# Performance work log

Hardware: AMD Instinct MI355X
Metric: run time of the kernel (lower is better)

The kernel has to match this reference:

```python
import jax, jax.numpy as jnp
import numpy as np

B = 2
N = 300000
C_IN = 2
PC = (-75.2, -75.2, 75.2, 75.2)
BEV = 0.8
GRID = int(round((PC[2] - PC[0]) / BEV))  # 188
CH = 256


def setup_inputs() -> dict:
    key = jax.random.key(0)
    ks = jax.random.split(key, 8)
    xy = jax.random.uniform(ks[0], (N, 2), minval=PC[0], maxval=PC[2], dtype=jnp.float32)
    z = jax.random.uniform(ks[1], (N, 1), minval=-2.0, maxval=4.0, dtype=jnp.float32)
    xyz = jnp.concatenate([xy, z], axis=-1)
    xyz_batch_cnt = jnp.full((B,), N // B, dtype=jnp.int32)
    pt_features = jax.random.normal(ks[2], (N, C_IN), dtype=jnp.float32)
    mlp_w = jax.random.normal(ks[3], (6 + C_IN, CH), dtype=jnp.float32) * 0.1
    mlp_g = jnp.ones((CH,), jnp.float32)
    mlp_b = jnp.zeros((CH,), jnp.float32)
    conv4_w = jax.random.normal(ks[4], (5, 3, 3, CH, CH), dtype=jnp.float32) * 0.02
    conv4_g = jnp.ones((5, CH), jnp.float32)
    conv4_b = jnp.zeros((5, CH), jnp.float32)
    conv5_w = jax.random.normal(ks[5], (5, 3, 3, CH, CH), dtype=jnp.float32) * 0.02
    conv5_g = jnp.ones((5, CH), jnp.float32)
    conv5_b = jnp.zeros((5, CH), jnp.float32)
    return dict(xyz=xyz, pt_features=pt_features, xyz_batch_cnt=xyz_batch_cnt,
                mlp_w=mlp_w, mlp_g=mlp_g, mlp_b=mlp_b,
                conv4_w=conv4_w, conv4_g=conv4_g, conv4_b=conv4_b,
                conv5_w=conv5_w, conv5_g=conv5_g, conv5_b=conv5_b)


def _conv(x, w, stride=1):
    # NHWC input, HWIO kernel, torch padding=1
    return jax.lax.conv_general_dilated(x, w, (stride, stride), [(1, 1), (1, 1)],
                                        dimension_numbers=("NHWC", "HWIO", "NHWC"))


def _bn(x, g, b):
    # eval-mode BatchNorm folded into per-channel affine
    return x * g + b


def _forward(xyz, pt_features, xyz_batch_cnt, mlp_w, mlp_g, mlp_b,
             conv4_w, conv4_g, conv4_b, conv5_w, conv5_g, conv5_b):
    n = xyz.shape[0]
    batch_idx = jnp.repeat(jnp.arange(B, dtype=jnp.int32), xyz_batch_cnt, total_repeat_length=n)
    ix = jnp.clip(jnp.floor((xyz[:, 0] - PC[0]) / BEV).astype(jnp.int32), 0, GRID - 1)
    iy = jnp.clip(jnp.floor((xyz[:, 1] - PC[1]) / BEV).astype(jnp.int32), 0, GRID - 1)
    cx = PC[0] + (ix.astype(xyz.dtype) + 0.5) * BEV
    cy = PC[1] + (iy.astype(xyz.dtype) + 0.5) * BEV
    # 6 geometric features (xyz + offsets to pillar center) + raw point features
    feat = jnp.concatenate([xyz,
                            (xyz[:, 0] - cx)[:, None],
                            (xyz[:, 1] - cy)[:, None],
                            xyz[:, 2:3],
                            pt_features], axis=-1)  # [N, 8]
    h = jax.nn.relu(_bn(feat @ mlp_w, mlp_g, mlp_b))  # [N, 256]
    flat = (batch_idx * GRID + iy) * GRID + ix  # [N]
    grid = jnp.full((B * GRID * GRID, CH), -jnp.inf, h.dtype).at[flat].max(h)
    occ = jnp.zeros((B * GRID * GRID, 1), h.dtype).at[flat].set(1.0)
    x = jnp.where(occ > 0, grid, 0.0).reshape(B, GRID, GRID, CH)
    mask = occ.reshape(B, GRID, GRID, 1)
    relu = jax.nn.relu
    # Sparse2DBasicBlockV (submanifold convs == dense conv on zero-padded grid + active-site mask)
    x0 = mask * relu(_bn(_conv(x, conv4_w[0]), conv4_g[0], conv4_b[0]))
    out = mask * relu(_bn(_conv(x0, conv4_w[1]), conv4_g[1], conv4_b[1]))
    out = mask * _bn(_conv(out, conv4_w[2]), conv4_g[2], conv4_b[2])
    x1 = relu(out + x0)
    # Sparse2DBasicBlock
    out = mask * relu(_bn(_conv(x1, conv4_w[3]), conv4_g[3], conv4_b[3]))
    out = mask * _bn(_conv(out, conv4_w[4]), conv4_g[4], conv4_b[4])
    x_conv4 = relu(out + x1)  # [B, 188, 188, 256]
    # conv5: strided dense conv + 2 Dense2DBasicBlocks
    y = relu(_bn(_conv(x_conv4, conv5_w[0], stride=2), conv5_g[0], conv5_b[0]))  # [B, 94, 94, 256]
    for i in (1, 3):
        out = relu(_bn(_conv(y, conv5_w[i]), conv5_g[i], conv5_b[i]))
        out = _bn(_conv(out, conv5_w[i + 1]), conv5_g[i + 1], conv5_b[i + 1])
        y = relu(out + y)
    return (jnp.transpose(x_conv4, (0, 3, 1, 2)), jnp.transpose(y, (0, 3, 1, 2)))


def reference(xyz, pt_features, xyz_batch_cnt, mlp_w, mlp_g, mlp_b,
              conv4_w, conv4_g, conv4_b, conv5_w, conv5_g, conv5_b):
    return _forward(xyz, pt_features, xyz_batch_cnt, mlp_w, mlp_g, mlp_b,
                    conv4_w, conv4_g, conv4_b, conv5_w, conv5_g, conv5_b)
```

## Files before the change

### kernel.cpp

```cpp
#include <hip/hip_runtime.h>
#include <hip/hip_bf16.h>


typedef __attribute__((ext_vector_type(8))) short bf16x8;
typedef __attribute__((ext_vector_type(4))) float f32x4;
typedef unsigned short u16;

#define GLD16(g, l)                                                   \
    __builtin_amdgcn_global_load_lds(                                 \
        (const __attribute__((address_space(1))) void*)(g),           \
        (__attribute__((address_space(3))) void*)(l), 16, 0, 0)

__device__ __forceinline__ u16 f2b(float f) {
    unsigned u = __float_as_uint(f);
    u += 0x7fffu + ((u >> 16) & 1u);
    return (u16)(u >> 16);
}
__device__ __forceinline__ float b2f(u16 h) {
    return __uint_as_float(((unsigned)h) << 16);
}

__global__ __launch_bounds__(256) void bin_kernel(
    const float* __restrict__ xyz, const int* __restrict__ cnt,
    int* __restrict__ pcnt, int* __restrict__ plist, int N) {
    int i = blockIdx.x * 256 + threadIdx.x;
    if (i >= N) return;
    float x = xyz[3 * i], y = xyz[3 * i + 1];
    int b = (i < cnt[0]) ? 0 : 1;
    int ix = (int)floorf((x + 75.2f) / 0.8f);
    int iy = (int)floorf((y + 75.2f) / 0.8f);
    ix = min(max(ix, 0), 187);
    iy = min(max(iy, 0), 187);
    int flat = (b * 188 + iy) * 188 + ix;
    int slot = atomicAdd(pcnt + flat, 1);
    if (slot < 32) plist[flat * 32 + slot] = i;
}

__global__ __launch_bounds__(256) void pillar_kernel(
    const float* __restrict__ xyz, const float* __restrict__ ptf,
    const float* __restrict__ mw, const float* __restrict__ mg,
    const float* __restrict__ mb, const int* __restrict__ pcnt,
    const int* __restrict__ plist, u16* __restrict__ out,
    float* __restrict__ occ) {
    const int lane = threadIdx.x & 63, wid = threadIdx.x >> 6;
    const int p = blockIdx.x * 4 + wid;
    const int n = min(pcnt[p], 32);
    const int c = lane * 4;
    float m0 = 0.f, m1 = 0.f, m2 = 0.f, m3 = 0.f;
    if (n > 0) {
        const int ix = p % 188;
        const int iy = (p / 188) % 188;
        const float cx = -75.2f + ((float)ix + 0.5f) * 0.8f;
        const float cy = -75.2f + ((float)iy + 0.5f) * 0.8f;
        float4 w[8];
#pragma unroll
        for (int k = 0; k < 8; k++) w[k] = *(const float4*)(mw + k * 256 + c);
        for (int t = 0; t < n; t++) {
            int i = __builtin_amdgcn_readfirstlane(plist[p * 32 + t]);
            float x = xyz[3 * i], y = xyz[3 * i + 1], z = xyz[3 * i + 2];
            float f0 = ptf[2 * i], f1 = ptf[2 * i + 1];
            const float f[8] = {x, y, z, x - cx, y - cy, z, f0, f1};
            float s0 = 0.f, s1 = 0.f, s2 = 0.f, s3 = 0.f;
#pragma unroll
            for (int k = 0; k < 8; k++) {
                s0 = fmaf(f[k], w[k].x, s0);
                s1 = fmaf(f[k], w[k].y, s1);
                s2 = fmaf(f[k], w[k].z, s2);
                s3 = fmaf(f[k], w[k].w, s3);
            }
            float4 g4 = *(const float4*)(mg + c);
            float4 b4 = *(const float4*)(mb + c);
            m0 = fmaxf(m0, fmaxf(s0 * g4.x + b4.x, 0.f));
            m1 = fmaxf(m1, fmaxf(s1 * g4.y + b4.y, 0.f));
            m2 = fmaxf(m2, fmaxf(s2 * g4.z + b4.z, 0.f));
            m3 = fmaxf(m3, fmaxf(s3 * g4.w + b4.w, 0.f));
        }
    }
    unsigned lo = (unsigned)f2b(m0) | ((unsigned)f2b(m1) << 16);
    unsigned hi = (unsigned)f2b(m2) | ((unsigned)f2b(m3) << 16);
    *(uint2*)(out + (size_t)p * 256 + c) = make_uint2(lo, hi);
    if (lane == 0) occ[p] = (n > 0) ? 1.f : 0.f;
}

__global__ void cvt_weights_kernel(const float* __restrict__ w4,
                                   const float* __restrict__ w5,
                                   u16* __restrict__ wt4,
                                   u16* __restrict__ wt5) {
    int bid = blockIdx.x;
    int mat = bid >> 4;
    int tile = bid & 15;
    int tr = tile >> 2, tc = tile & 3;
    const float* src = (mat < 45) ? (w4 + (size_t)mat * 65536)
                                  : (w5 + (size_t)(mat - 45) * 65536);
    u16* dst = (mat < 45) ? (wt4 + (size_t)mat * 65536)
                          : (wt5 + (size_t)(mat - 45) * 65536);
    __shared__ u16 sm[64][65];
    int tx = threadIdx.x & 63, ty = threadIdx.x >> 6;
#pragma unroll
    for (int k = 0; k < 64; k += 4) {
        int c = tr * 64 + ty + k;
        int n = tc * 64 + tx;
        sm[tx][ty + k] = f2b(src[c * 256 + n]);
    }
    __syncthreads();
#pragma unroll
    for (int k = 0; k < 64; k += 4) {
        int n = tc * 64 + ty + k;
        int c = tr * 64 + tx;
        dst[n * 256 + c] = sm[ty + k][tx];
    }
}

template <int STRIDE, bool HAS_MASK, bool HAS_RES, bool HAS_F32OUT>
__global__ __launch_bounds__(256) void conv3x3_kernel(
    const u16* __restrict__ in,
    const u16* __restrict__ wt,
    const u16* __restrict__ zeros,
    const float* __restrict__ gamma, const float* __restrict__ beta,
    const float* __restrict__ mask, const u16* __restrict__ res,
    u16* __restrict__ outb, float* __restrict__ outf,
    int Hin, int Win, int Hout, int Wout, int Bn) {
    const int M = Bn * Hout * Wout;
    const int HWo = Hout * Wout;
    const int HWi = Hin * Win;
    const int tid = threadIdx.x;
    const int lane = tid & 63, wid = tid >> 6;
    const int wr = wid >> 1, wc = wid & 1;

    const int nwg = gridDim.x;
    const int q = nwg >> 3, r = nwg & 7;
    const int xc = blockIdx.x & 7, jj = blockIdx.x >> 3;
    const int wg = (xc < r ? xc * (q + 1) : r * (q + 1) + (xc - r) * q) + jj;
    const int m0 = (wg >> 1) * 128;
    const int n0 = (wg & 1) * 128;

    __shared__ u16 SMEM[32768];

    const int lrow = lane >> 3;
    const int csw = (((lane & 7) ^ (lrow & 7)) << 3);

    int ppy[4], ppx[4], ppb[4];
    bool ppo[4];
#pragma unroll
    for (int j = 0; j < 4; j++) {
        int gp = m0 + wid * 32 + j * 8 + lrow;
        ppo[j] = gp < M;
        int g2 = ppo[j] ? gp : 0;
        int b = g2 / HWo;
        int rr = g2 - b * HWo;
        ppy[j] = rr / Wout;
        ppx[j] = rr - ppy[j] * Wout;
        ppb[j] = b;
    }
    int bofs[4];
#pragma unroll
    for (int j = 0; j < 4; j++)
        bofs[j] = (n0 + wid * 32 + j * 8 + lrow) * 256 + csw;

#define MKPTR(dst, T)                                                         \
    do {                                                                      \
        int dy_ = (T) / 3 - 1, dx_ = (T) % 3 - 1;                             \
        _Pragma("unroll") for (int j = 0; j < 4; j++) {                       \
            int sy_ = ppy[j] * STRIDE + dy_;                                  \
            int sx_ = ppx[j] * STRIDE + dx_;                                  \
            bool ok_ = ppo[j] && sy_ >= 0 && sy_ < Hin && sx_ >= 0 &&         \
                       sx_ < Win;                                             \
            long long off_ =                                                  \
                ((long long)ppb[j] * HWi + (long long)sy_ * Win + sx_) * 256; \
            dst[j] = ok_ ? in + off_ + csw : zeros + csw;                     \
        }                                                                     \
    } while (0)

#define ISSUE(APTR, T, KC, BUF)                                               \
    do {                                                                      \
        u16* dA_ = SMEM + (BUF)*16384;                                        \
        u16* dB_ = dA_ + 8192;                                                \
        _Pragma("unroll") for (int j = 0; j < 4; j++) {                       \
            GLD16(APTR[j] + (KC)*64, dA_ + (wid * 32 + j * 8) * 64);          \
            GLD16(wt + (T)*65536 + bofs[j] + (KC)*64,                         \
                  dB_ + (wid * 32 + j * 8) * 64);                             \
        }                                                                     \
    } while (0)

    f32x4 acc[4][4];
#pragma unroll
    for (int m = 0; m < 4; m++)
#pragma unroll
        for (int n = 0; n < 4; n++) acc[m][n] = (f32x4)0.f;

    const u16* aptrc[4];
    const u16* aptrn[4];
    MKPTR(aptrc, 0);
    ISSUE(aptrc, 0, 0, 0);

    const int rA = lane & 15;
    const int kb = (lane >> 4) * 8;
    const int xk = (rA & 7) << 3;

#pragma unroll 1
    for (int t = 0; t < 9; t++) {
        MKPTR(aptrn, t + 1);
#pragma unroll
        for (int kc = 0; kc < 4; kc++) {
            asm volatile("s_waitcnt vmcnt(0)" ::: "memory");
            __builtin_amdgcn_sched_barrier(0);
            __builtin_amdgcn_s_barrier();
            __builtin_amdgcn_sched_barrier(0);
            if (kc < 3) {
                ISSUE(aptrc, t, kc + 1, (kc + 1) & 1);
            } else if (t < 8) {
                ISSUE(aptrn, t + 1, 0, 0);
            }
            __builtin_amdgcn_sched_barrier(0);
            const u16* Ar = SMEM + (kc & 1) * 16384;
            const u16* Br = Ar + 8192;
#pragma unroll
            for (int kh = 0; kh < 2; kh++) {
                bf16x8 af[4], bfr[4];
#pragma unroll
                for (int m = 0; m < 4; m++)
                    af[m] = *(const bf16x8*)(Ar + (wr * 64 + m * 16 + rA) * 64 +
                                             ((kh * 32 + kb) ^ xk));
#pragma unroll
                for (int n = 0; n < 4; n++)
                    bfr[n] = *(const bf16x8*)(Br + (wc * 64 + n * 16 + rA) * 64 +
                                              ((kh * 32 + kb) ^ xk));
                __builtin_amdgcn_s_setprio(1);
#pragma unroll
                for (int m = 0; m < 4; m++)
#pragma unroll
                    for (int n = 0; n < 4; n++)
                        acc[m][n] = __builtin_amdgcn_mfma_f32_16x16x32_bf16(
                            af[m], bfr[n], acc[m][n], 0, 0, 0);
                __builtin_amdgcn_s_setprio(0);
            }
        }
#pragma unroll
        for (int j = 0; j < 4; j++) aptrc[j] = aptrn[j];
    }

    float* ep = (float*)SMEM + wid * 2048;
    const int cb = n0 + wc * 64;
    float gms[4], bts[4];
#pragma unroll
    for (int n = 0; n < 4; n++) {
        gms[n] = gamma[cb + n * 16 + (lane & 15)];
        bts[n] = beta[cb + n * 16 + (lane & 15)];
    }
#pragma unroll
    for (int half = 0; half < 2; half++) {
#pragma unroll
        for (int m2 = 0; m2 < 2; m2++) {
            const int m = half * 2 + m2;
            const int lrb = m2 * 16 + ((lane >> 4) << 2);
            const int gpb = m0 + wr * 64 + half * 32 + lrb;
#pragma unroll
            for (int rr = 0; rr < 4; rr++) {
                float mk = 1.f;
                if (HAS_MASK) mk = (gpb + rr < M) ? mask[gpb + rr] : 0.f;
#pragma unroll
                for (int n = 0; n < 4; n++) {
                    float v = acc[m][n][rr] * gms[n] + bts[n];
                    if (HAS_MASK) v *= mk;
                    ep[(lrb + rr) * 64 + n * 16 + (lane & 15)] = v;
                }
            }
        }
#pragma unroll
        for (int i = 0; i < 8; i++) {
            const int lr = i * 4 + (lane >> 4);
            const int gp = m0 + wr * 64 + half * 32 + lr;
            f32x4 v = *(const f32x4*)(ep + lr * 64 + (lane & 15) * 4);
            if (HAS_RES && gp < M) {
                uint2 rv = *(const uint2*)(res + (size_t)gp * 256 + cb + (lane & 15) * 4);
                v[0] += b2f((u16)(rv.x & 0xffff));
                v[1] += b2f((u16)(rv.x >> 16));
                v[2] += b2f((u16)(rv.y & 0xffff));
                v[3] += b2f((u16)(rv.y >> 16));
            }
            v[0] = fmaxf(v[0], 0.f);
            v[1] = fmaxf(v[1], 0.f);
            v[2] = fmaxf(v[2], 0.f);
            v[3] = fmaxf(v[3], 0.f);
            if (HAS_F32OUT)
                *(f32x4*)(ep + lr * 64 + (lane & 15) * 4) = v;
            if (gp < M) {
                unsigned lo = (unsigned)f2b(v[0]) | ((unsigned)f2b(v[1]) << 16);
                unsigned hi = (unsigned)f2b(v[2]) | ((unsigned)f2b(v[3]) << 16);
                *(uint2*)(outb + (size_t)gp * 256 + cb + (lane & 15) * 4) =
                    make_uint2(lo, hi);
            }
        }
        if (HAS_F32OUT) {
#pragma unroll
            for (int i = 0; i < 16; i++) {
                const int lc = i * 4 + (lane >> 4);
                const int p0 = (lane & 15) * 2;
                const int gp0 = m0 + wr * 64 + half * 32 + p0;
                if (gp0 < M) {
                    float v0 = ep[p0 * 64 + lc];
                    float v1 = ep[(p0 + 1) * 64 + lc];
                    int b = gp0 / HWo;
                    int rr = gp0 - b * HWo;
                    const int ch = cb + lc;
                    float* o = outf + ((size_t)(b * 256 + ch)) * HWo + rr;
                    *(float2*)o = make_float2(v0, v1);
                }
            }
        }
    }
#undef MKPTR
#undef ISSUE
}

extern "C" void kernel_launch(void* const* d_in, const int* in_sizes, int n_in,
                              void* d_out, int out_size, void* d_ws,
                              size_t ws_size, hipStream_t stream) {
    const float* xyz = (const float*)d_in[0];
    const float* ptf = (const float*)d_in[1];
    const int* cnt = (const int*)d_in[2];
    const float* mw = (const float*)d_in[3];
    const float* mg = (const float*)d_in[4];
    const float* mb = (const float*)d_in[5];
    const float* c4w = (const float*)d_in[6];
    const float* c4g = (const float*)d_in[7];
    const float* c4b = (const float*)d_in[8];
    const float* c5w = (const float*)d_in[9];
    const float* c5g = (const float*)d_in[10];
    const float* c5b = (const float*)d_in[11];
    const int N = in_sizes[0] / 3;

    char* ws = (char*)d_ws;
    int* pcnt = (int*)ws;
    u16* zeros = (u16*)(ws + 282752);
    float* occ = (float*)(ws + 283264);
    int* plist = (int*)(ws + 566016);
    u16* wt4 = (u16*)(ws + 9614080);
    u16* wt5 = (u16*)(ws + 15512320);
    u16* bufA = (u16*)(ws + 21410560);
    u16* bufB = (u16*)(ws + 57602816);
    u16* bufC = (u16*)(ws + 93795072);

    float* outXC4 = (float*)d_out;
    float* outY = ((float*)d_out) + 18096128;

    const int M188 = 2 * 188 * 188;
    const int M94 = 2 * 94 * 94;

    hipMemsetAsync(ws, 0, 283264, stream);
    cvt_weights_kernel<<<90 * 16, 256, 0, stream>>>(c4w, c5w, wt4, wt5);
    bin_kernel<<<(N + 255) / 256, 256, 0, stream>>>(xyz, cnt, pcnt, plist, N);
    pillar_kernel<<<M188 / 4, 256, 0, stream>>>(xyz, ptf, mw, mg, mb, pcnt,
                                                plist, bufA, occ);

    dim3 g188(2 * ((M188 + 127) / 128)), g94(2 * ((M94 + 127) / 128));
    const size_t WL = 9 * 65536;

    conv3x3_kernel<1, true, false, false><<<g188, 256, 0, stream>>>(
        bufA, wt4 + 0 * WL, zeros, c4g + 0, c4b + 0, occ, nullptr, bufB,
        nullptr, 188, 188, 188, 188, 2);
    conv3x3_kernel<1, true, false, false><<<g188, 256, 0, stream>>>(
        bufB, wt4 + 1 * WL, zeros, c4g + 256, c4b + 256, occ, nullptr, bufC,
        nullptr, 188, 188, 188, 188, 2);
    conv3x3_kernel<1, true, true, false><<<g188, 256, 0, stream>>>(
        bufC, wt4 + 2 * WL, zeros, c4g + 512, c4b + 512, occ, bufB, bufA,
        nullptr, 188, 188, 188, 188, 2);
    conv3x3_kernel<1, true, false, false><<<g188, 256, 0, stream>>>(
        bufA, wt4 + 3 * WL, zeros, c4g + 768, c4b + 768, occ, nullptr, bufC,
        nullptr, 188, 188, 188, 188, 2);
    conv3x3_kernel<1, true, true, true><<<g188, 256, 0, stream>>>(
        bufC, wt4 + 4 * WL, zeros, c4g + 1024, c4b + 1024, occ, bufA, bufB,
        outXC4, 188, 188, 188, 188, 2);

    conv3x3_kernel<2, false, false, false><<<g94, 256, 0, stream>>>(
        bufB, wt5 + 0 * WL, zeros, c5g + 0, c5b + 0, nullptr, nullptr, bufA,
        nullptr, 188, 188, 94, 94, 2);
    conv3x3_kernel<1, false, false, false><<<g94, 256, 0, stream>>>(
        bufA, wt5 + 1 * WL, zeros, c5g + 256, c5b + 256, nullptr, nullptr,
        bufC, nullptr, 94, 94, 94, 94, 2);
    conv3x3_kernel<1, false, true, false><<<g94, 256, 0, stream>>>(
        bufC, wt5 + 2 * WL, zeros, c5g + 512, c5b + 512, nullptr, bufA, bufB,
        nullptr, 94, 94, 94, 94, 2);
    conv3x3_kernel<1, false, false, false><<<g94, 256, 0, stream>>>(
        bufB, wt5 + 3 * WL, zeros, c5g + 768, c5b + 768, nullptr, nullptr,
        bufC, nullptr, 94, 94, 94, 94, 2);
    conv3x3_kernel<1, false, true, true><<<g94, 256, 0, stream>>>(
        bufC, wt5 + 4 * WL, zeros, c5g + 1024, c5b + 1024, nullptr, bufB,
        bufA, outY, 94, 94, 94, 94, 2);
}
```

Before: 838.0 us.

## Add halo-tiled stride-1 conv kernel reusing LDS input tile across 3x3 taps

Adds a new stride-1 3x3 conv kernel that tiles output as 2 rows by 64 columns. It loads the 4x66 input halo tile (per 64-channel chunk) into LDS once and reuses it for all nine taps, instead of re-gathering im2col rows for each tap. Weights are streamed from global memory straight into registers with double buffering, and the kernel requests 2 blocks per CU via launch bounds. This cuts redundant input loads and LDS traffic. The cost is extra register pressure and wasted work on the partial column tiles (188 and 94 are not multiples of 64). The strided conv keeps the old kernel, which now gets a barrier before its epilogue.

```diff
diff --git a/kernel.cpp b/kernel.cpp
--- a/kernel.cpp
+++ b/kernel.cpp
@@ -111,22 +111,195 @@
     }
 }
 
-template <int STRIDE, bool HAS_MASK, bool HAS_RES, bool HAS_F32OUT>
-__global__ __launch_bounds__(256) void conv3x3_kernel(
+template <bool HAS_MASK, bool HAS_RES, bool HAS_F32OUT>
+__global__ __launch_bounds__(256, 2) void conv3x3_halo_kernel(
     const u16* __restrict__ in,
     const u16* __restrict__ wt,
     const u16* __restrict__ zeros,
     const float* __restrict__ gamma, const float* __restrict__ beta,
     const float* __restrict__ mask, const u16* __restrict__ res,
     u16* __restrict__ outb, float* __restrict__ outf,
-    int Hin, int Win, int Hout, int Wout, int Bn) {
+    int H, int W, int tx, int ty) {
+    const int tid = threadIdx.x;
+    const int lane = tid & 63, wid = tid >> 6;
+    const int wr = wid >> 1, wc = wid & 1;
+    const int rA = lane & 15, kq = lane >> 4;
+
+    const int nwg = gridDim.x;
+    const int q = nwg >> 3, r = nwg & 7;
+    const int xcd = blockIdx.x & 7, jj = blockIdx.x >> 3;
+    int wg = (xcd < r ? xcd * (q + 1) : r * (q + 1) + (xcd - r) * q) + jj;
+    const int nh = wg & 1;
+    int t2 = wg >> 1;
+    const int txi = t2 % tx;
+    t2 /= tx;
+    const int tyi = t2 % ty;
+    const int bimg = t2 / ty;
+    const int x0 = txi * 64, y0 = tyi * 2, n0 = nh * 128;
+
+    __shared__ u16 SMEM[18432];
+
+    const u16* sbase[9];
+#pragma unroll
+    for (int i = 0; i < 9; i++) {
+        int g = i * 256 + tid;
+        int rr_ = g / 576;
+        int rem = g - rr_ * 576;
+        int c_ = rem >> 3;
+        int k8 = rem & 7;
+        int yi = y0 - 1 + rr_;
+        int xi = x0 - 1 + c_;
+        bool ok = (yi >= 0) && (yi < H) && (xi >= 0) && (xi < W);
+        int k8s = (k8 ^ (c_ & 7)) * 8;
+        sbase[i] = ok ? in + ((size_t)(bimg * H + yi) * W + xi) * 256 + k8s
+                      : zeros + k8s;
+    }
+    const u16* bptr[4];
+#pragma unroll
+    for (int nf = 0; nf < 4; nf++)
+        bptr[nf] = wt + (size_t)(n0 + wc * 64 + nf * 16 + rA) * 256 + kq * 8;
+
+    f32x4 acc[4][4];
+#pragma unroll
+    for (int m = 0; m < 4; m++)
+#pragma unroll
+        for (int n = 0; n < 4; n++) acc[m][n] = (f32x4)0.f;
+
+#pragma unroll 1
+    for (int cc = 0; cc < 4; cc++) {
+        __builtin_amdgcn_s_barrier();
+#pragma unroll
+        for (int i = 0; i < 9; i++)
+            GLD16(sbase[i] + cc * 64, SMEM + (i * 256 + wid * 64) * 8);
+        bf16x8 bfr[2][8];
+#pragma unroll
+        for (int nf = 0; nf < 4; nf++)
+#pragma unroll
+            for (int kh = 0; kh < 2; kh++)
+                bfr[0][nf * 2 + kh] =
+                    *(const bf16x8*)(bptr[nf] + cc * 64 + kh * 32);
+        __syncthreads();
+#pragma unroll
+        for (int t = 0; t < 9; t++) {
+            if (t < 8) {
+#pragma unroll
+                for (int nf = 0; nf < 4; nf++)
+#pragma unroll
+                    for (int kh = 0; kh < 2; kh++)
+                        bfr[(t + 1) & 1][nf * 2 + kh] = *(const bf16x8*)(
+                            bptr[nf] + (t + 1) * 65536 + cc * 64 + kh * 32);
+            }
+            const int dy = t / 3 - 1, dx = t % 3 - 1;
+            bf16x8 af[4][2];
+#pragma unroll
+            for (int m = 0; m < 4; m++) {
+                int hc = m * 16 + rA + 1 + dx;
+                int rowb = (((wr + 1 + dy) * 72 + hc) << 6);
+                int xv = hc & 7;
+#pragma unroll
+                for (int kh = 0; kh < 2; kh++)
+                    af[m][kh] = *(const bf16x8*)(
+                        SMEM + rowb + (((kh << 2) + kq) ^ xv) * 8);
+            }
+            __builtin_amdgcn_s_setprio(1);
+#pragma unroll
+            for (int kh = 0; kh < 2; kh++)
+#pragma unroll
+                for (int m = 0; m < 4; m++)
+#pragma unroll
+                    for (int nf = 0; nf < 4; nf++)
+                        acc[m][nf] = __builtin_amdgcn_mfma_f32_16x16x32_bf16(
+                            af[m][kh], bfr[t & 1][nf * 2 + kh], acc[m][nf],
+                            0, 0, 0);
+            __builtin_amdgcn_s_setprio(0);
+        }
+    }
+
+    __builtin_amdgcn_s_barrier();
+    float* ep = (float*)SMEM + wid * 2048;
+    const int cb = n0 + wc * 64;
+    const int row = y0 + wr;
+    const size_t gprow = (size_t)(bimg * H + row) * W;
+    float gms[4], bts[4];
+#pragma unroll
+    for (int n = 0; n < 4; n++) {
+        gms[n] = gamma[cb + n * 16 + rA];
+        bts[n] = beta[cb + n * 16 + rA];
+    }
+#pragma unroll
+    for (int half = 0; half < 2; half++) {
+#pragma unroll
+        for (int m2 = 0; m2 < 2; m2++) {
+            const int m = half * 2 + m2;
+            const int lrb = m2 * 16 + (kq << 2);
+#pragma unroll
+            for (int rr = 0; rr < 4; rr++) {
+                const int col = x0 + half * 32 + lrb + rr;
+                float mk = 1.f;
+                if (HAS_MASK) mk = (col < W) ? mask[gprow + col] : 0.f;
+#pragma unroll
+                for (int n = 0; n < 4; n++) {
+                    float v = acc[m][n][rr] * gms[n] + bts[n];
+                    if (HAS_MASK) v *= mk;
+                    ep[(lrb + rr) * 64 + n * 16 + rA] = v;
+                }
+            }
+        }
+#pragma unroll
+        for (int i = 0; i < 8; i++) {
+            const int lr = i * 4 + kq;
+            const int col = x0 + half * 32 + lr;
+            const size_t gp = gprow + col;
+            f32x4 v = *(const f32x4*)(ep + lr * 64 + rA * 4);
+            if (HAS_RES && col < W) {
+                uint2 rv = *(const uint2*)(res + gp * 256 + cb + rA * 4);
+                v[0] += b2f((u16)(rv.x & 0xffff));
+                v[1] += b2f((u16)(rv.x >> 16));
+                v[2] += b2f((u16)(rv.y & 0xffff));
+                v[3] += b2f((u16)(rv.y >> 16));
+            }
+            v[0] = fmaxf(v[0], 0.f);
+            v[1] = fmaxf(v[1], 0.f);
+            v[2] = fmaxf(v[2], 0.f);
+            v[3] = fmaxf(v[3], 0.f);
+            if (HAS_F32OUT) *(f32x4*)(ep + lr * 64 + rA * 4) = v;
+            if (col < W) {
+                unsigned lo = (unsigned)f2b(v[0]) | ((unsigned)f2b(v[1]) << 16);
+                unsigned hi = (unsigned)f2b(v[2]) | ((unsigned)f2b(v[3]) << 16);
+                *(uint2*)(outb + gp * 256 + cb + rA * 4) = make_uint2(lo, hi);
+            }
+        }
+        if (HAS_F32OUT) {
+#pragma unroll
+            for (int i = 0; i < 16; i++) {
+                const int lc = i * 4 + kq;
+                const int px0 = rA * 2;
+                const int col0 = x0 + half * 32 + px0;
+                if (col0 < W) {
+                    float v0 = ep[px0 * 64 + lc];
+                    float v1 = ep[(px0 + 1) * 64 + lc];
+                    const int ch = cb + lc;
+                    float* o = outf + ((size_t)(bimg * 256 + ch) * H + row) * W + col0;
+                    *(float2*)o = make_float2(v0, v1);
+                }
+            }
+        }
+    }
+}
+
+template <int STRIDE, bool HAS_MASK, bool HAS_RES, bool HAS_F32OUT>
+__global__ __launch_bounds__(256) void conv3x3_kernel(
+    const u16* __restrict__ in, const u16* __restrict__ wt,
+    const u16* __restrict__ zeros, const float* __restrict__ gamma,
+    const float* __restrict__ beta, const float* __restrict__ mask,
+    const u16* __restrict__ res, u16* __restrict__ outb,
+    float* __restrict__ outf, int Hin, int Win, int Hout, int Wout, int Bn) {
     const int M = Bn * Hout * Wout;
     const int HWo = Hout * Wout;
     const int HWi = Hin * Win;
     const int tid = threadIdx.x;
     const int lane = tid & 63, wid = tid >> 6;
     const int wr = wid >> 1, wc = wid & 1;
-
     const int nwg = gridDim.x;
     const int q = nwg >> 3, r = nwg & 7;
     const int xc = blockIdx.x & 7, jj = blockIdx.x >> 3;
@@ -135,7 +308,6 @@
     const int n0 = (wg & 1) * 128;
 
     __shared__ u16 SMEM[32768];
-
     const int lrow = lane >> 3;
     const int csw = (((lane & 7) ^ (lrow & 7)) << 3);
 
@@ -239,6 +411,7 @@
         for (int j = 0; j < 4; j++) aptrc[j] = aptrn[j];
     }
 
+    __syncthreads();
     float* ep = (float*)SMEM + wid * 2048;
     const int cb = n0 + wc * 64;
     float gms[4], bts[4];
@@ -282,8 +455,7 @@
             v[1] = fmaxf(v[1], 0.f);
             v[2] = fmaxf(v[2], 0.f);
             v[3] = fmaxf(v[3], 0.f);
-            if (HAS_F32OUT)
-                *(f32x4*)(ep + lr * 64 + (lane & 15) * 4) = v;
+            if (HAS_F32OUT) *(f32x4*)(ep + lr * 64 + (lane & 15) * 4) = v;
             if (gp < M) {
                 unsigned lo = (unsigned)f2b(v[0]) | ((unsigned)f2b(v[1]) << 16);
                 unsigned hi = (unsigned)f2b(v[2]) | ((unsigned)f2b(v[3]) << 16);
@@ -344,47 +516,48 @@
     float* outXC4 = (float*)d_out;
     float* outY = ((float*)d_out) + 18096128;
 
-    const int M188 = 2 * 188 * 188;
     const int M94 = 2 * 94 * 94;
 
     hipMemsetAsync(ws, 0, 283264, stream);
     cvt_weights_kernel<<<90 * 16, 256, 0, stream>>>(c4w, c5w, wt4, wt5);
     bin_kernel<<<(N + 255) / 256, 256, 0, stream>>>(xyz, cnt, pcnt, plist, N);
-    pillar_kernel<<<M188 / 4, 256, 0, stream>>>(xyz, ptf, mw, mg, mb, pcnt,
-                                                plist, bufA, occ);
-
-    dim3 g188(2 * ((M188 + 127) / 128)), g94(2 * ((M94 + 127) / 128));
+    pillar_kernel<<<(2 * 188 * 188) / 4, 256, 0, stream>>>(
+        xyz, ptf, mw, mg, mb, pcnt, plist, bufA, occ);
+
+    dim3 gh188(3 * 94 * 2 * 2);
+    dim3 gh94(2 * 47 * 2 * 2);
+    dim3 g94s2(2 * ((M94 + 127) / 128));
     const size_t WL = 9 * 65536;
 
-    conv3x3_kernel<1, true, false, false><<<g188, 256, 0, stream>>>(
+    conv3x3_halo_kernel<true, false, false><<<gh188, 256, 0, stream>>>(
         bufA, wt4 + 0 * WL, zeros, c4g + 0, c4b + 0, occ, nullptr, bufB,
-        nullptr, 188, 188, 188, 188, 2);
-    conv3x3_kernel<1, true, false, false><<<g188, 256, 0, stream>>>(
+        nullptr, 188, 188, 3, 94);
+    conv3x3_halo_kernel<true, false, false><<<gh188, 256, 0, stream>>>(
         bufB, wt4 + 1 * WL, zeros, c4g + 256, c4b + 256, occ, nullptr, bufC,
-        nullptr, 188, 188, 188, 188, 2);
-    conv3x3_kernel<1, true, true, false><<<g188, 256, 0, stream>>>(
+        nullptr, 188, 188, 3, 94);
+    conv3x3_halo_kernel<true, true, false><<<gh188, 256, 0, stream>>>(
         bufC, wt4 + 2 * WL, zeros, c4g + 512, c4b + 512, occ, bufB, bufA,
-        nullptr, 188, 188, 188, 188, 2);
-    conv3x3_kernel<1, true, false, false><<<g188, 256, 0, stream>>>(
+        nullptr, 188, 188, 3, 94);
+    conv3x3_halo_kernel<true, false, false><<<gh188, 256, 0, stream>>>(
         bufA, wt4 + 3 * WL, zeros, c4g + 768, c4b + 768, occ, nullptr, bufC,
-        nullptr, 188, 188, 188, 188, 2);
-    conv3x3_kernel<1, true, true, true><<<g188, 256, 0, stream>>>(
+        nullptr, 188, 188, 3, 94);
+    conv3x3_halo_kernel<true, true, true><<<gh188, 256, 0, stream>>>(
         bufC, wt4 + 4 * WL, zeros, c4g + 1024, c4b + 1024, occ, bufA, bufB,
-        outXC4, 188, 188, 188, 188, 2);
-
-    conv3x3_kernel<2, false, false, false><<<g94, 256, 0, stream>>>(
+        outXC4, 188, 188, 3, 94);
+
+    conv3x3_kernel<2, false, false, false><<<g94s2, 256, 0, stream>>>(
         bufB, wt5 + 0 * WL, zeros, c5g + 0, c5b + 0, nullptr, nullptr, bufA,
         nullptr, 188, 188, 94, 94, 2);
-    conv3x3_kernel<1, false, false, false><<<g94, 256, 0, stream>>>(
+    conv3x3_halo_kernel<false, false, false><<<gh94, 256, 0, stream>>>(
         bufA, wt5 + 1 * WL, zeros, c5g + 256, c5b + 256, nullptr, nullptr,
-        bufC, nullptr, 94, 94, 94, 94, 2);
-    conv3x3_kernel<1, false, true, false><<<g94, 256, 0, stream>>>(
+        bufC, nullptr, 94, 94, 2, 47);
+    conv3x3_halo_kernel<false, true, false><<<gh94, 256, 0, stream>>>(
         bufC, wt5 + 2 * WL, zeros, c5g + 512, c5b + 512, nullptr, bufA, bufB,
-        nullptr, 94, 94, 94, 94, 2);
-    conv3x3_kernel<1, false, false, false><<<g94, 256, 0, stream>>>(
+        nullptr, 94, 94, 2, 47);
+    conv3x3_halo_kernel<false, false, false><<<gh94, 256, 0, stream>>>(
         bufB, wt5 + 3 * WL, zeros, c5g + 768, c5b + 768, nullptr, nullptr,
-        bufC, nullptr, 94, 94, 94, 94, 2);
-    conv3x3_kernel<1, false, true, true><<<g94, 256, 0, stream>>>(
+        bufC, nullptr, 94, 94, 2, 47);
+    conv3x3_halo_kernel<false, true, true><<<gh94, 256, 0, stream>>>(
         bufC, wt5 + 4 * WL, zeros, c5g + 1024, c5b + 1024, nullptr, bufB,
-        bufA, outY, 94, 94, 94, 94, 2);
-}
+        bufA, outY, 94, 94, 2, 47);
+}
```

After: 1.391 ms. +66.0%, slower.

## Triple-buffer conv3x3 LDS pipeline and pad epilogue staging rows

Applied to the files above, without the earlier changes.

Moves the conv3x3 main loop from double to triple LDS buffering. The next chunk's global-to-LDS loads are now issued before the barrier, and the wait is a partial vmcnt(8), so loads for one stage can overlap the MFMA work of the current stage instead of draining fully each step. The epilogue staging rows are padded from 64 to 66 floats to cut LDS bank conflicts, with a syncthreads added before that reuse. The cost is 96KB of LDS per block, which can reduce resident blocks per CU, and padded rows leave some 16-byte vector LDS accesses misaligned.

```diff
diff --git a/kernel.cpp b/kernel.cpp
--- a/kernel.cpp
+++ b/kernel.cpp
@@ -113,20 +113,17 @@
 
 template <int STRIDE, bool HAS_MASK, bool HAS_RES, bool HAS_F32OUT>
 __global__ __launch_bounds__(256) void conv3x3_kernel(
-    const u16* __restrict__ in,
-    const u16* __restrict__ wt,
-    const u16* __restrict__ zeros,
-    const float* __restrict__ gamma, const float* __restrict__ beta,
-    const float* __restrict__ mask, const u16* __restrict__ res,
-    u16* __restrict__ outb, float* __restrict__ outf,
-    int Hin, int Win, int Hout, int Wout, int Bn) {
+    const u16* __restrict__ in, const u16* __restrict__ wt,
+    const u16* __restrict__ zeros, const float* __restrict__ gamma,
+    const float* __restrict__ beta, const float* __restrict__ mask,
+    const u16* __restrict__ res, u16* __restrict__ outb,
+    float* __restrict__ outf, int Hin, int Win, int Hout, int Wout, int Bn) {
     const int M = Bn * Hout * Wout;
     const int HWo = Hout * Wout;
     const int HWi = Hin * Win;
     const int tid = threadIdx.x;
     const int lane = tid & 63, wid = tid >> 6;
     const int wr = wid >> 1, wc = wid & 1;
-
     const int nwg = gridDim.x;
     const int q = nwg >> 3, r = nwg & 7;
     const int xc = blockIdx.x & 7, jj = blockIdx.x >> 3;
@@ -134,8 +131,7 @@
     const int m0 = (wg >> 1) * 128;
     const int n0 = (wg & 1) * 128;
 
-    __shared__ u16 SMEM[32768];
-
+    __shared__ u16 SMEM[49152];
     const int lrow = lane >> 3;
     const int csw = (((lane & 7) ^ (lrow & 7)) << 3);
 
@@ -196,23 +192,32 @@
     const int rA = lane & 15;
     const int kb = (lane >> 4) * 8;
     const int xk = (rA & 7) << 3;
+    int b0 = 0;
 
 #pragma unroll 1
     for (int t = 0; t < 9; t++) {
         MKPTR(aptrn, t + 1);
 #pragma unroll
         for (int kc = 0; kc < 4; kc++) {
-            asm volatile("s_waitcnt vmcnt(0)" ::: "memory");
+            int ib = b0 + kc;
+            if (ib >= 3) ib -= 3;
+            int ibn = ib + 1;
+            if (ibn >= 3) ibn -= 3;
+            if (kc < 3) {
+                ISSUE(aptrc, t, kc + 1, ibn);
+            } else if (t < 8) {
+                ISSUE(aptrn, t + 1, 0, ibn);
+            }
+            __builtin_amdgcn_sched_barrier(0);
+            if (kc < 3 || t < 8) {
+                asm volatile("s_waitcnt vmcnt(8)" ::: "memory");
+            } else {
+                asm volatile("s_waitcnt vmcnt(0)" ::: "memory");
+            }
             __builtin_amdgcn_sched_barrier(0);
             __builtin_amdgcn_s_barrier();
             __builtin_amdgcn_sched_barrier(0);
-            if (kc < 3) {
-                ISSUE(aptrc, t, kc + 1, (kc + 1) & 1);
-            } else if (t < 8) {
-                ISSUE(aptrn, t + 1, 0, 0);
-            }
-            __builtin_amdgcn_sched_barrier(0);
-            const u16* Ar = SMEM + (kc & 1) * 16384;
+            const u16* Ar = SMEM + ib * 16384;
             const u16* Br = Ar + 8192;
 #pragma unroll
             for (int kh = 0; kh < 2; kh++) {
@@ -237,15 +242,17 @@
         }
 #pragma unroll
         for (int j = 0; j < 4; j++) aptrc[j] = aptrn[j];
-    }
-
-    float* ep = (float*)SMEM + wid * 2048;
+        b0 = (b0 == 2) ? 0 : b0 + 1;
+    }
+
+    __syncthreads();
+    float* ep = (float*)SMEM + wid * 2112;
     const int cb = n0 + wc * 64;
     float gms[4], bts[4];
 #pragma unroll
     for (int n = 0; n < 4; n++) {
-        gms[n] = gamma[cb + n * 16 + (lane & 15)];
-        bts[n] = beta[cb + n * 16 + (lane & 15)];
+        gms[n] = gamma[cb + n * 16 + rA];
+        bts[n] = beta[cb + n * 16 + rA];
     }
 #pragma unroll
     for (int half = 0; half < 2; half++) {
@@ -262,7 +269,7 @@
                 for (int n = 0; n < 4; n++) {
                     float v = acc[m][n][rr] * gms[n] + bts[n];
                     if (HAS_MASK) v *= mk;
-                    ep[(lrb + rr) * 64 + n * 16 + (lane & 15)] = v;
+                    ep[(lrb + rr) * 66 + n * 16 + rA] = v;
                 }
             }
         }
@@ -270,9 +277,9 @@
         for (int i = 0; i < 8; i++) {
             const int lr = i * 4 + (lane >> 4);
             const int gp = m0 + wr * 64 + half * 32 + lr;
-            f32x4 v = *(const f32x4*)(ep + lr * 64 + (lane & 15) * 4);
+            f32x4 v = *(const f32x4*)(ep + lr * 66 + rA * 4);
             if (HAS_RES && gp < M) {
-                uint2 rv = *(const uint2*)(res + (size_t)gp * 256 + cb + (lane & 15) * 4);
+                uint2 rv = *(const uint2*)(res + (size_t)gp * 256 + cb + rA * 4);
                 v[0] += b2f((u16)(rv.x & 0xffff));
                 v[1] += b2f((u16)(rv.x >> 16));
                 v[2] += b2f((u16)(rv.y & 0xffff));
@@ -282,12 +289,11 @@
             v[1] = fmaxf(v[1], 0.f);
             v[2] = fmaxf(v[2], 0.f);
             v[3] = fmaxf(v[3], 0.f);
-            if (HAS_F32OUT)
-                *(f32x4*)(ep + lr * 64 + (lane & 15) * 4) = v;
+            if (HAS_F32OUT) *(f32x4*)(ep + lr * 66 + rA * 4) = v;
             if (gp < M) {
                 unsigned lo = (unsigned)f2b(v[0]) | ((unsigned)f2b(v[1]) << 16);
                 unsigned hi = (unsigned)f2b(v[2]) | ((unsigned)f2b(v[3]) << 16);
-                *(uint2*)(outb + (size_t)gp * 256 + cb + (lane & 15) * 4) =
+                *(uint2*)(outb + (size_t)gp * 256 + cb + rA * 4) =
                     make_uint2(lo, hi);
             }
         }
@@ -295,11 +301,11 @@
 #pragma unroll
             for (int i = 0; i < 16; i++) {
                 const int lc = i * 4 + (lane >> 4);
-                const int p0 = (lane & 15) * 2;
+                const int p0 = rA * 2;
                 const int gp0 = m0 + wr * 64 + half * 32 + p0;
                 if (gp0 < M) {
-                    float v0 = ep[p0 * 64 + lc];
-                    float v1 = ep[(p0 + 1) * 64 + lc];
+                    float v0 = ep[p0 * 66 + lc];
+                    float v1 = ep[(p0 + 1) * 66 + lc];
                     int b = gp0 / HWo;
                     int rr = gp0 - b * HWo;
                     const int ch = cb + lc;
```

New measurement: 1.190 ms. 42.0% more time.
